# Optimization experiments

Measured on AMD Instinct MI355X. Metric: run time of the kernel, lower is better.

Reference implementation:

```python
import jax, jax.numpy as jnp
import numpy as np

D_MODEL = 1024
NUM_HEADS = 16
D_HEAD = D_MODEL // NUM_HEADS


def setup_inputs() -> dict:
    key = jax.random.key(0)
    ks = jax.random.split(key, 11)
    B, S = 2, 2048
    s = 1.0 / np.sqrt(D_MODEL)
    inp = {
        "Q": jax.random.normal(ks[0], (B, S, D_MODEL), dtype=jnp.float32),
        "K": jax.random.normal(ks[1], (B, S, D_MODEL), dtype=jnp.float32),
        "V": jax.random.normal(ks[2], (B, S, D_MODEL), dtype=jnp.float32),
        "W_q": jax.random.normal(ks[3], (D_MODEL, D_MODEL), dtype=jnp.float32) * s,
        "b_q": jnp.zeros((D_MODEL,), dtype=jnp.float32),
        "W_k": jax.random.normal(ks[4], (D_MODEL, D_MODEL), dtype=jnp.float32) * s,
        "b_k": jnp.zeros((D_MODEL,), dtype=jnp.float32),
        "W_v": jax.random.normal(ks[5], (D_MODEL, D_MODEL), dtype=jnp.float32) * s,
        "b_v": jnp.zeros((D_MODEL,), dtype=jnp.float32),
        "W_o": jax.random.normal(ks[6], (D_MODEL, D_MODEL), dtype=jnp.float32) * s,
        "b_o": jnp.zeros((D_MODEL,), dtype=jnp.float32),
    }
    return inp


def reference(Q, K, V, W_q, b_q, W_k, b_k, W_v, b_v, W_o, b_o):
    B, S, _ = Q.shape
    # Linear projections (torch Linear: x @ W.T + b)
    q = Q @ W_q.T + b_q  # [B,S,D]
    k = K @ W_k.T + b_k
    v = V @ W_v.T + b_v
    # split heads -> [B,H,S,d]
    q = q.reshape(B, S, NUM_HEADS, D_HEAD).transpose(0, 2, 1, 3)
    k = k.reshape(B, S, NUM_HEADS, D_HEAD).transpose(0, 2, 1, 3)
    v = v.reshape(B, S, NUM_HEADS, D_HEAD).transpose(0, 2, 1, 3)
    scores = jnp.einsum("bhqd,bhkd->bhqk", q, k) / np.sqrt(D_HEAD).astype(np.float32)
    attn = jax.nn.softmax(scores, axis=-1)
    out = jnp.einsum("bhqk,bhkd->bhqd", attn, v)
    out = out.transpose(0, 2, 1, 3).reshape(B, S, D_MODEL)
    return out @ W_o.T + b_o
```

## Files before the change

kernel.cpp:

```cpp
#include <hip/hip_runtime.h>
#include <stdint.h>

#define D_MODEL 1024
#define S_LEN   2048
#define BATCH   2
#define NHEAD   16
#define DHEAD   64
#define NTOK    (BATCH * S_LEN)

typedef unsigned short u16;
typedef __attribute__((ext_vector_type(8))) short bf16x8;
typedef __attribute__((ext_vector_type(4))) float f32x4;
typedef __attribute__((ext_vector_type(16))) float f32x16;
typedef __attribute__((ext_vector_type(2))) unsigned int u32x2;

__device__ __forceinline__ unsigned pack2bf(float lo, float hi) {
    unsigned a = __float_as_uint(lo) + 0x8000u;
    unsigned b = __float_as_uint(hi) + 0x8000u;
    return __builtin_amdgcn_perm(b, a, 0x07060302u);
}
__device__ __forceinline__ u16 f2bf1(float f) {
    return (u16)((__float_as_uint(f) + 0x8000u) >> 16);
}

#define GAS(p) ((const __attribute__((address_space(1))) void*)(p))
#define LAS(p) ((__attribute__((address_space(3))) void*)(p))
#define SWZ8(row, c) (((((row) << 3) | ((c) ^ ((row) & 7)))) << 3)

__global__ __launch_bounds__(256) void convert_kernel(
    const float* __restrict__ Q, const float* __restrict__ K, const float* __restrict__ V,
    const float* __restrict__ Wq, const float* __restrict__ Wk,
    const float* __restrict__ Wv, const float* __restrict__ Wo,
    u16* __restrict__ Qb, u16* __restrict__ Kb, u16* __restrict__ Vb,
    u16* __restrict__ Wqb, u16* __restrict__ Wkb, u16* __restrict__ Wvb, u16* __restrict__ Wob)
{
    const size_t SEG = 262144;
    size_t start = (size_t)blockIdx.x * 4096;
    int s = (int)(start / SEG);
    const float* src; u16* dst; size_t seg0;
    if (s < 4)       { src = Q;  dst = Qb;  seg0 = 0; }
    else if (s < 8)  { src = K;  dst = Kb;  seg0 = 4 * SEG; }
    else if (s < 12) { src = V;  dst = Vb;  seg0 = 8 * SEG; }
    else if (s == 12){ src = Wq; dst = Wqb; seg0 = 12 * SEG; }
    else if (s == 13){ src = Wk; dst = Wkb; seg0 = 13 * SEG; }
    else if (s == 14){ src = Wv; dst = Wvb; seg0 = 14 * SEG; }
    else             { src = Wo; dst = Wob; seg0 = 15 * SEG; }
    size_t off = start - seg0 + threadIdx.x;
    const float4* s4 = (const float4*)src;
    #pragma unroll
    for (int k = 0; k < 16; ++k) {
        float4 x = s4[off + (size_t)k * 256];
        u32x2 p = (u32x2){pack2bf(x.x, x.y), pack2bf(x.z, x.w)};
        *(u32x2*)(dst + (off + (size_t)k * 256) * 4) = p;
    }
}

__global__ __launch_bounds__(256) void proj_kernel(
    const u16* __restrict__ Qb, const u16* __restrict__ Kb, const u16* __restrict__ Vb,
    const u16* __restrict__ Wqb, const u16* __restrict__ Wkb, const u16* __restrict__ Wvb,
    const float* __restrict__ bq, const float* __restrict__ bk, const float* __restrict__ bv,
    u16* __restrict__ qw, u16* __restrict__ kw, u16* __restrict__ vtw)
{
    const int z = blockIdx.z;
    const int bx = blockIdx.x;
    const u16* A = (z == 0) ? Wqb : (z == 1) ? Wkb : Wvb;
    const u16* B = (z == 0) ? Qb  : (z == 1) ? Kb  : Vb;
    const float* bias = (z == 0) ? bq : (z == 1) ? bk : bv;
    const int mbase = (bx & 7) * 128;
    const int nbase = (bx >> 3) * 128;

    const int tid = threadIdx.x, lane = tid & 63, wave = tid >> 6;
    const int m16 = lane & 15, quad = lane >> 4;
    const int wm = wave >> 1, wn = wave & 1;

    __shared__ __align__(16) u16 As[128 * 64];
    __shared__ __align__(16) u16 Bs[128 * 64];

    int srow[4], scg[4];
    #pragma unroll
    for (int c = 0; c < 4; ++c) {
        int p = (wave * 4 + c) * 64 + lane;
        srow[c] = p >> 3;
        scg[c]  = (p & 7) ^ (srow[c] & 7);
    }

    f32x4 acc[4][4];
    #pragma unroll
    for (int mt = 0; mt < 4; ++mt)
        #pragma unroll
        for (int nt = 0; nt < 4; ++nt) acc[mt][nt] = (f32x4){0.f, 0.f, 0.f, 0.f};

    for (int kc = 0; kc < D_MODEL; kc += 64) {
        #pragma unroll
        for (int c = 0; c < 4; ++c) {
            __builtin_amdgcn_global_load_lds(
                GAS(A + (size_t)(mbase + srow[c]) * D_MODEL + kc + scg[c] * 8),
                LAS(As + (wave * 4 + c) * 512), 16, 0, 0);
            __builtin_amdgcn_global_load_lds(
                GAS(B + (size_t)(nbase + srow[c]) * D_MODEL + kc + scg[c] * 8),
                LAS(Bs + (wave * 4 + c) * 512), 16, 0, 0);
        }
        __syncthreads();
        #pragma unroll
        for (int half = 0; half < 2; ++half) {
            bf16x8 af[4], bfr[4];
            #pragma unroll
            for (int mt = 0; mt < 4; ++mt)
                af[mt] = *(const bf16x8*)&As[SWZ8(wm * 64 + mt * 16 + m16, quad + 4 * half)];
            #pragma unroll
            for (int nt = 0; nt < 4; ++nt)
                bfr[nt] = *(const bf16x8*)&Bs[SWZ8(wn * 64 + nt * 16 + m16, quad + 4 * half)];
            #pragma unroll
            for (int mt = 0; mt < 4; ++mt)
                #pragma unroll
                for (int nt = 0; nt < 4; ++nt)
                    acc[mt][nt] = __builtin_amdgcn_mfma_f32_16x16x32_bf16(af[mt], bfr[nt], acc[mt][nt], 0, 0, 0);
        }
        __syncthreads();
    }

    if (z < 2) {
        u16* Y = z ? kw : qw;
        const float scale = z ? 1.0f : 0.18033688011112042f;
        #pragma unroll
        for (int mt = 0; mt < 4; ++mt) {
            int d0 = mbase + wm * 64 + mt * 16 + quad * 4;
            float4 b4 = *(const float4*)&bias[d0];
            #pragma unroll
            for (int nt = 0; nt < 4; ++nt) {
                int tok = nbase + wn * 64 + nt * 16 + m16;
                float v0 = (acc[mt][nt][0] + b4.x) * scale;
                float v1 = (acc[mt][nt][1] + b4.y) * scale;
                float v2 = (acc[mt][nt][2] + b4.z) * scale;
                float v3 = (acc[mt][nt][3] + b4.w) * scale;
                *(u32x2*)(Y + (size_t)tok * D_MODEL + d0) =
                    (u32x2){pack2bf(v0, v1), pack2bf(v2, v3)};
            }
        }
    } else {
        #pragma unroll
        for (int mt = 0; mt < 4; ++mt)
            #pragma unroll
            for (int r = 0; r < 4; ++r) {
                int dout = mbase + wm * 64 + mt * 16 + quad * 4 + r;
                float bb = bias[dout];
                #pragma unroll
                for (int nt = 0; nt < 4; ++nt) {
                    int tok = nbase + wn * 64 + nt * 16 + m16;
                    vtw[(size_t)dout * NTOK + tok] = f2bf1(acc[mt][nt][r] + bb);
                }
            }
    }
}

__global__ __launch_bounds__(512, 4) void attn_kernel(
    const u16* __restrict__ qw, const u16* __restrict__ kw,
    const u16* __restrict__ vtw, u16* __restrict__ aw)
{
    const int qbase = blockIdx.x * 128;
    const int h = blockIdx.y, b = blockIdx.z;
    const int tid = threadIdx.x, lane = tid & 63, wave = tid >> 6;
    const int wq = wave & 3;
    const int wk = wave >> 2;
    const int l31 = lane & 31;
    const int hh  = lane >> 5;
    const int colbase = h * DHEAD;
    const size_t qrow0 = (size_t)b * S_LEN + qbase;

    __shared__ __align__(16) u16 smem[17664];
    #define KS_OFF(buf) ((buf) * 4096)
    #define VS_OFF(buf) (8192 + (buf) * 4096)

    const int srow = tid >> 3;
    const int scg  = (tid & 7) ^ (srow & 7);
    const size_t ksrc = ((size_t)b * S_LEN + srow) * D_MODEL + colbase + scg * 8;
    const size_t vsrc = (size_t)(colbase + srow) * NTOK + (size_t)b * S_LEN + scg * 8;

    #define STAGE_KV(buf, kv0)                                                         \
        do {                                                                           \
            __builtin_amdgcn_global_load_lds(GAS(kw + ksrc + (size_t)(kv0) * D_MODEL), \
                                             LAS(smem + KS_OFF(buf) + wave * 512), 16, 0, 0); \
            __builtin_amdgcn_global_load_lds(GAS(vtw + vsrc + (kv0)),                  \
                                             LAS(smem + VS_OFF(buf) + wave * 512), 16, 0, 0); \
        } while (0)

    bf16x8 qf[4];
    {
        const u16* qptr = qw + (qrow0 + wq * 32 + l31) * D_MODEL + colbase + hh * 8;
        #pragma unroll
        for (int s = 0; s < 4; ++s) qf[s] = *(const bf16x8*)(qptr + s * 16);
    }

    STAGE_KV(0, 0);

    f32x16 o[2];
    #pragma unroll
    for (int dt = 0; dt < 2; ++dt)
        #pragma unroll
        for (int r = 0; r < 16; ++r) o[dt][r] = 0.f;
    float l = 0.f;

    __syncthreads();

    for (int t = 0; t < S_LEN / 64; ++t) {
        const int cur = t & 1;
        if (t + 1 < S_LEN / 64) STAGE_KV(!cur, (t + 1) * 64);

        f32x16 sc;
        #pragma unroll
        for (int r = 0; r < 16; ++r) sc[r] = -12.f;
        #pragma unroll
        for (int s = 0; s < 4; ++s) {
            bf16x8 kf = *(const bf16x8*)&smem[KS_OFF(cur) + SWZ8(wk * 32 + l31, s * 2 + hh)];
            sc = __builtin_amdgcn_mfma_f32_32x32x16_bf16(kf, qf[s], sc, 0, 0, 0);
        }

        unsigned x[4][2], y[4][2];
        #pragma unroll
        for (int g = 0; g < 4; ++g) {
            float p0 = __builtin_amdgcn_exp2f(sc[4 * g + 0]);
            float p1 = __builtin_amdgcn_exp2f(sc[4 * g + 1]);
            float p2 = __builtin_amdgcn_exp2f(sc[4 * g + 2]);
            float p3 = __builtin_amdgcn_exp2f(sc[4 * g + 3]);
            l += (p0 + p1) + (p2 + p3);
            x[g][0] = pack2bf(p0, p1);
            x[g][1] = pack2bf(p2, p3);
        }
        #pragma unroll
        for (int g = 0; g < 4; ++g) {
            y[g][0] = __shfl_xor((int)x[g][0], 32);
            y[g][1] = __shfl_xor((int)x[g][1], 32);
        }

        #pragma unroll
        for (int sp = 0; sp < 2; ++sp) {
            const int ge = 2 * sp, go = 2 * sp + 1;
            union { unsigned u[4]; bf16x8 v; } pf;
            pf.u[0] = hh ? y[go][0] : x[ge][0];
            pf.u[1] = hh ? y[go][1] : x[ge][1];
            pf.u[2] = hh ? x[go][0] : y[ge][0];
            pf.u[3] = hh ? x[go][1] : y[ge][1];
            #pragma unroll
            for (int dt = 0; dt < 2; ++dt) {
                bf16x8 vf = *(const bf16x8*)&smem[VS_OFF(cur) + SWZ8(dt * 32 + l31, wk * 4 + sp * 2 + hh)];
                o[dt] = __builtin_amdgcn_mfma_f32_32x32x16_bf16(vf, pf.v, o[dt], 0, 0, 0);
            }
        }

        __syncthreads();
    }

    l += __shfl_xor(l, 32);

    float* Ored = (float*)smem;
    float* Lred = (float*)(smem + 17408);
    float* op = Ored + ((size_t)wq * 32 + l31) * 68;
    if (wk == 1) {
        #pragma unroll
        for (int dt = 0; dt < 2; ++dt)
            #pragma unroll
            for (int g = 0; g < 4; ++g)
                *(f32x4*)(op + dt * 32 + 8 * g + 4 * hh) =
                    (f32x4){o[dt][4 * g + 0], o[dt][4 * g + 1], o[dt][4 * g + 2], o[dt][4 * g + 3]};
        if (hh == 0) Lred[wq * 32 + l31] = l;
    }
    __syncthreads();
    if (wk == 0) {
        l += Lred[wq * 32 + l31];
        float inv = 1.0f / l;
        size_t orow = (qrow0 + wq * 32 + l31) * D_MODEL + colbase;
        #pragma unroll
        for (int dt = 0; dt < 2; ++dt)
            #pragma unroll
            for (int g = 0; g < 4; ++g) {
                f32x4 add = *(const f32x4*)(op + dt * 32 + 8 * g + 4 * hh);
                float v0 = (o[dt][4 * g + 0] + add[0]) * inv;
                float v1 = (o[dt][4 * g + 1] + add[1]) * inv;
                float v2 = (o[dt][4 * g + 2] + add[2]) * inv;
                float v3 = (o[dt][4 * g + 3] + add[3]) * inv;
                *(u32x2*)(aw + orow + dt * 32 + 8 * g + 4 * hh) =
                    (u32x2){pack2bf(v0, v1), pack2bf(v2, v3)};
            }
    }
    #undef STAGE_KV
    #undef KS_OFF
    #undef VS_OFF
}

__global__ __launch_bounds__(256) void outproj_kernel(
    const u16* __restrict__ aw, const u16* __restrict__ Wob,
    const float* __restrict__ bo, float* __restrict__ out)
{
    const int nbase = blockIdx.x * 64;
    const int mbase = blockIdx.y * 128;
    const int tid = threadIdx.x, lane = tid & 63, wave = tid >> 6;
    const int m16 = lane & 15, quad = lane >> 4;
    const int wm = wave >> 1, wn = wave & 1;

    __shared__ __align__(16) u16 As[128 * 64];
    __shared__ __align__(16) u16 Bs[64 * 64];

    int arow[4], acg[4], brow[2], bcg[2];
    #pragma unroll
    for (int c = 0; c < 4; ++c) {
        int p = (wave * 4 + c) * 64 + lane;
        arow[c] = p >> 3; acg[c] = (p & 7) ^ (arow[c] & 7);
    }
    #pragma unroll
    for (int c = 0; c < 2; ++c) {
        int p = (wave * 2 + c) * 64 + lane;
        brow[c] = p >> 3; bcg[c] = (p & 7) ^ (brow[c] & 7);
    }

    f32x4 acc[4][2];
    #pragma unroll
    for (int mt = 0; mt < 4; ++mt)
        #pragma unroll
        for (int nt = 0; nt < 2; ++nt) acc[mt][nt] = (f32x4){0.f, 0.f, 0.f, 0.f};

    for (int kc = 0; kc < D_MODEL; kc += 64) {
        #pragma unroll
        for (int c = 0; c < 4; ++c)
            __builtin_amdgcn_global_load_lds(
                GAS(Wob + (size_t)(mbase + arow[c]) * D_MODEL + kc + acg[c] * 8),
                LAS(As + (wave * 4 + c) * 512), 16, 0, 0);
        #pragma unroll
        for (int c = 0; c < 2; ++c)
            __builtin_amdgcn_global_load_lds(
                GAS(aw + (size_t)(nbase + brow[c]) * D_MODEL + kc + bcg[c] * 8),
                LAS(Bs + (wave * 2 + c) * 512), 16, 0, 0);
        __syncthreads();
        #pragma unroll
        for (int half = 0; half < 2; ++half) {
            bf16x8 af[4], bfr[2];
            #pragma unroll
            for (int mt = 0; mt < 4; ++mt)
                af[mt] = *(const bf16x8*)&As[SWZ8(wm * 64 + mt * 16 + m16, quad + 4 * half)];
            #pragma unroll
            for (int nt = 0; nt < 2; ++nt)
                bfr[nt] = *(const bf16x8*)&Bs[SWZ8(wn * 32 + nt * 16 + m16, quad + 4 * half)];
            #pragma unroll
            for (int mt = 0; mt < 4; ++mt)
                #pragma unroll
                for (int nt = 0; nt < 2; ++nt)
                    acc[mt][nt] = __builtin_amdgcn_mfma_f32_16x16x32_bf16(af[mt], bfr[nt], acc[mt][nt], 0, 0, 0);
        }
        __syncthreads();
    }

    #pragma unroll
    for (int mt = 0; mt < 4; ++mt) {
        int d0 = mbase + wm * 64 + mt * 16 + quad * 4;
        float4 b4 = *(const float4*)&bo[d0];
        #pragma unroll
        for (int nt = 0; nt < 2; ++nt) {
            int tok = nbase + wn * 32 + nt * 16 + m16;
            float4 st;
            st.x = acc[mt][nt][0] + b4.x;
            st.y = acc[mt][nt][1] + b4.y;
            st.z = acc[mt][nt][2] + b4.z;
            st.w = acc[mt][nt][3] + b4.w;
            *(float4*)(out + (size_t)tok * D_MODEL + d0) = st;
        }
    }
}

extern "C" void kernel_launch(void* const* d_in, const int* in_sizes, int n_in,
                              void* d_out, int out_size, void* d_ws, size_t ws_size,
                              hipStream_t stream) {
    const float* Q  = (const float*)d_in[0];
    const float* K  = (const float*)d_in[1];
    const float* V  = (const float*)d_in[2];
    const float* Wq = (const float*)d_in[3];
    const float* bq = (const float*)d_in[4];
    const float* Wk = (const float*)d_in[5];
    const float* bk = (const float*)d_in[6];
    const float* Wv = (const float*)d_in[7];
    const float* bv = (const float*)d_in[8];
    const float* Wo = (const float*)d_in[9];
    const float* bo = (const float*)d_in[10];

    const size_t NT = (size_t)NTOK * D_MODEL;
    const size_t WN = (size_t)D_MODEL * D_MODEL;
    u16* base = (u16*)d_ws;
    u16* qw  = base;
    u16* kw  = base + NT;
    u16* vtw = base + 2 * NT;
    u16* Qb  = base + 3 * NT;
    u16* Kb  = base + 4 * NT;
    u16* Vb  = base + 5 * NT;
    u16* Wqb = base + 6 * NT;
    u16* Wkb = Wqb + WN;
    u16* Wvb = Wkb + WN;
    u16* Wob = Wvb + WN;
    u16* aww = Qb;

    convert_kernel<<<1024, 256, 0, stream>>>(Q, K, V, Wq, Wk, Wv, Wo,
                                             Qb, Kb, Vb, Wqb, Wkb, Wvb, Wob);
    proj_kernel<<<dim3(256, 1, 3), 256, 0, stream>>>(Qb, Kb, Vb, Wqb, Wkb, Wvb,
                                                     bq, bk, bv, qw, kw, vtw);
    attn_kernel<<<dim3(S_LEN / 128, NHEAD, BATCH), 512, 0, stream>>>(qw, kw, vtw, aww);
    outproj_kernel<<<dim3(NTOK / 64, D_MODEL / 128), 256, 0, stream>>>(
        aww, Wob, bo, (float*)d_out);
}
```

Measured before the change: 228.4 us.

## Enlarge projection GEMM tiles to 256x256 with double-buffered LDS and 32x32 MFMA

Restructures the QKV projection GEMM to compute 256x256 tiles per 512-thread block, using 32x32x16 bf16 MFMAs and a two-stage LDS buffer. The next K-chunk is prefetched via global_load_lds while the current one is computed. Blocks are remapped so related tiles land on the same XCD. This aims to raise data reuse and overlap memory with compute, at the cost of a 128 KB LDS footprint, one block per CU and only 192 blocks, fewer than the CU count.

```diff
diff --git a/kernel.cpp b/kernel.cpp
--- a/kernel.cpp
+++ b/kernel.cpp
@@ -55,99 +55,120 @@
     }
 }
 
-__global__ __launch_bounds__(256) void proj_kernel(
+__global__ __launch_bounds__(512, 2) void proj_kernel(
     const u16* __restrict__ Qb, const u16* __restrict__ Kb, const u16* __restrict__ Vb,
     const u16* __restrict__ Wqb, const u16* __restrict__ Wkb, const u16* __restrict__ Wvb,
     const float* __restrict__ bq, const float* __restrict__ bk, const float* __restrict__ bv,
     u16* __restrict__ qw, u16* __restrict__ kw, u16* __restrict__ vtw)
 {
-    const int z = blockIdx.z;
-    const int bx = blockIdx.x;
-    const u16* A = (z == 0) ? Wqb : (z == 1) ? Wkb : Wvb;
-    const u16* B = (z == 0) ? Qb  : (z == 1) ? Kb  : Vb;
+    const int bid = blockIdx.x;
+    const int wid = (bid & 7) * 24 + (bid >> 3);
+    const int z = wid >> 6;
+    const int r = wid & 63;
+    const int nbase = (r >> 2) * 256;
+    const int mbase = (r & 3) * 256;
+
+    const u16* Ag = (z == 0) ? Wqb : (z == 1) ? Wkb : Wvb;
+    const u16* Bg = (z == 0) ? Qb  : (z == 1) ? Kb  : Vb;
     const float* bias = (z == 0) ? bq : (z == 1) ? bk : bv;
-    const int mbase = (bx & 7) * 128;
-    const int nbase = (bx >> 3) * 128;
 
     const int tid = threadIdx.x, lane = tid & 63, wave = tid >> 6;
-    const int m16 = lane & 15, quad = lane >> 4;
-    const int wm = wave >> 1, wn = wave & 1;
-
-    __shared__ __align__(16) u16 As[128 * 64];
-    __shared__ __align__(16) u16 Bs[128 * 64];
-
-    int srow[4], scg[4];
+    const int l31 = lane & 31, hh = lane >> 5;
+    const int wm = wave >> 2;
+    const int wn = wave & 3;
+
+    __shared__ __align__(16) u16 smem[65536];
+
+    size_t aoff[4], boff[4];
     #pragma unroll
     for (int c = 0; c < 4; ++c) {
         int p = (wave * 4 + c) * 64 + lane;
-        srow[c] = p >> 3;
-        scg[c]  = (p & 7) ^ (srow[c] & 7);
-    }
-
-    f32x4 acc[4][4];
+        int row = p >> 3;
+        int cg  = (p & 7) ^ (row & 7);
+        aoff[c] = (size_t)(mbase + row) * D_MODEL + cg * 8;
+        boff[c] = (size_t)(nbase + row) * D_MODEL + cg * 8;
+    }
+
+#define STAGE(buf, kc)                                                              \
+    do {                                                                            \
+        _Pragma("unroll")                                                           \
+        for (int c = 0; c < 4; ++c) {                                               \
+            __builtin_amdgcn_global_load_lds(GAS(Ag + aoff[c] + (kc)),              \
+                LAS(smem + (buf) * 16384 + (wave * 4 + c) * 512), 16, 0, 0);        \
+            __builtin_amdgcn_global_load_lds(GAS(Bg + boff[c] + (kc)),              \
+                LAS(smem + 32768 + (buf) * 16384 + (wave * 4 + c) * 512), 16, 0, 0);\
+        }                                                                           \
+    } while (0)
+
+    STAGE(0, 0);
+
+    f32x16 acc[4][2];
     #pragma unroll
     for (int mt = 0; mt < 4; ++mt)
         #pragma unroll
-        for (int nt = 0; nt < 4; ++nt) acc[mt][nt] = (f32x4){0.f, 0.f, 0.f, 0.f};
-
-    for (int kc = 0; kc < D_MODEL; kc += 64) {
-        #pragma unroll
-        for (int c = 0; c < 4; ++c) {
-            __builtin_amdgcn_global_load_lds(
-                GAS(A + (size_t)(mbase + srow[c]) * D_MODEL + kc + scg[c] * 8),
-                LAS(As + (wave * 4 + c) * 512), 16, 0, 0);
-            __builtin_amdgcn_global_load_lds(
-                GAS(B + (size_t)(nbase + srow[c]) * D_MODEL + kc + scg[c] * 8),
-                LAS(Bs + (wave * 4 + c) * 512), 16, 0, 0);
-        }
-        __syncthreads();
-        #pragma unroll
-        for (int half = 0; half < 2; ++half) {
-            bf16x8 af[4], bfr[4];
+        for (int nt = 0; nt < 2; ++nt)
+            #pragma unroll
+            for (int q = 0; q < 16; ++q) acc[mt][nt][q] = 0.f;
+
+    for (int t = 0; t < D_MODEL / 64; ++t) {
+        const int cur = t & 1;
+        asm volatile("s_waitcnt vmcnt(0) lgkmcnt(0)" ::: "memory");
+        __builtin_amdgcn_s_barrier();
+        asm volatile("" ::: "memory");
+        if (t < D_MODEL / 64 - 1) STAGE(cur ^ 1, (t + 1) * 64);
+        const u16* Ab = smem + cur * 16384;
+        const u16* Bb = smem + 32768 + cur * 16384;
+        #pragma unroll
+        for (int kk = 0; kk < 4; ++kk) {
+            bf16x8 af[4], bfr[2];
             #pragma unroll
             for (int mt = 0; mt < 4; ++mt)
-                af[mt] = *(const bf16x8*)&As[SWZ8(wm * 64 + mt * 16 + m16, quad + 4 * half)];
-            #pragma unroll
-            for (int nt = 0; nt < 4; ++nt)
-                bfr[nt] = *(const bf16x8*)&Bs[SWZ8(wn * 64 + nt * 16 + m16, quad + 4 * half)];
+                af[mt] = *(const bf16x8*)&Ab[SWZ8(wm * 128 + mt * 32 + l31, kk * 2 + hh)];
+            #pragma unroll
+            for (int nt = 0; nt < 2; ++nt)
+                bfr[nt] = *(const bf16x8*)&Bb[SWZ8(wn * 64 + nt * 32 + l31, kk * 2 + hh)];
             #pragma unroll
             for (int mt = 0; mt < 4; ++mt)
                 #pragma unroll
-                for (int nt = 0; nt < 4; ++nt)
-                    acc[mt][nt] = __builtin_amdgcn_mfma_f32_16x16x32_bf16(af[mt], bfr[nt], acc[mt][nt], 0, 0, 0);
-        }
-        __syncthreads();
-    }
+                for (int nt = 0; nt < 2; ++nt)
+                    acc[mt][nt] = __builtin_amdgcn_mfma_f32_32x32x16_bf16(af[mt], bfr[nt], acc[mt][nt], 0, 0, 0);
+        }
+    }
+#undef STAGE
 
     if (z < 2) {
         u16* Y = z ? kw : qw;
         const float scale = z ? 1.0f : 0.18033688011112042f;
         #pragma unroll
-        for (int mt = 0; mt < 4; ++mt) {
-            int d0 = mbase + wm * 64 + mt * 16 + quad * 4;
-            float4 b4 = *(const float4*)&bias[d0];
-            #pragma unroll
-            for (int nt = 0; nt < 4; ++nt) {
-                int tok = nbase + wn * 64 + nt * 16 + m16;
-                float v0 = (acc[mt][nt][0] + b4.x) * scale;
-                float v1 = (acc[mt][nt][1] + b4.y) * scale;
-                float v2 = (acc[mt][nt][2] + b4.z) * scale;
-                float v3 = (acc[mt][nt][3] + b4.w) * scale;
-                *(u32x2*)(Y + (size_t)tok * D_MODEL + d0) =
-                    (u32x2){pack2bf(v0, v1), pack2bf(v2, v3)};
+        for (int mt = 0; mt < 4; ++mt)
+            #pragma unroll
+            for (int nt = 0; nt < 2; ++nt) {
+                const int tok = nbase + wn * 64 + nt * 32 + l31;
+                u16* yrow = Y + (size_t)tok * D_MODEL;
+                #pragma unroll
+                for (int g = 0; g < 4; ++g) {
+                    const int d0 = mbase + wm * 128 + mt * 32 + 8 * g + 4 * hh;
+                    float4 b4 = *(const float4*)&bias[d0];
+                    float v0 = (acc[mt][nt][4 * g + 0] + b4.x) * scale;
+                    float v1 = (acc[mt][nt][4 * g + 1] + b4.y) * scale;
+                    float v2 = (acc[mt][nt][4 * g + 2] + b4.z) * scale;
+                    float v3 = (acc[mt][nt][4 * g + 3] + b4.w) * scale;
+                    *(u32x2*)(yrow + d0) = (u32x2){pack2bf(v0, v1), pack2bf(v2, v3)};
+                }
             }
-        }
     } else {
         #pragma unroll
         for (int mt = 0; mt < 4; ++mt)
             #pragma unroll
-            for (int r = 0; r < 4; ++r) {
-                int dout = mbase + wm * 64 + mt * 16 + quad * 4 + r;
-                float bb = bias[dout];
+            for (int nt = 0; nt < 2; ++nt) {
+                const int tok = nbase + wn * 64 + nt * 32 + l31;
                 #pragma unroll
-                for (int nt = 0; nt < 4; ++nt) {
-                    int tok = nbase + wn * 64 + nt * 16 + m16;
-                    vtw[(size_t)dout * NTOK + tok] = f2bf1(acc[mt][nt][r] + bb);
+                for (int g = 0; g < 4; ++g) {
+                    const int d0 = mbase + wm * 128 + mt * 32 + 8 * g + 4 * hh;
+                    #pragma unroll
+                    for (int q = 0; q < 4; ++q)
+                        vtw[(size_t)(d0 + q) * NTOK + tok] =
+                            f2bf1(acc[mt][nt][4 * g + q] + bias[d0 + q]);
                 }
             }
     }
@@ -397,8 +418,8 @@
 
     convert_kernel<<<1024, 256, 0, stream>>>(Q, K, V, Wq, Wk, Wv, Wo,
                                              Qb, Kb, Vb, Wqb, Wkb, Wvb, Wob);
-    proj_kernel<<<dim3(256, 1, 3), 256, 0, stream>>>(Qb, Kb, Vb, Wqb, Wkb, Wvb,
-                                                     bq, bk, bv, qw, kw, vtw);
+    proj_kernel<<<dim3(192), 512, 0, stream>>>(Qb, Kb, Vb, Wqb, Wkb, Wvb,
+                                               bq, bk, bv, qw, kw, vtw);
     attn_kernel<<<dim3(S_LEN / 128, NHEAD, BATCH), 512, 0, stream>>>(qw, kw, vtw, aww);
     outproj_kernel<<<dim3(NTOK / 64, D_MODEL / 128), 256, 0, stream>>>(
         aww, Wob, bo, (float*)d_out);
```

Result: faster. 219.1 us (-4.1%).
